# Optimization experiments

Measured on AMD Instinct MI355X. Metric: run time of the kernel, lower is better.

## Reference

```python
import jax, jax.numpy as jnp
import numpy as np

HEAD_SIZE = 64
TOKEN_EMB = 768
BLOCK_SIZE = 4096


def setup_inputs() -> dict:
    key = jax.random.key(0)
    ks = jax.random.split(key, 7)
    s = 1.0 / np.sqrt(TOKEN_EMB)  # torch Linear default init scale
    x = jax.random.normal(ks[0], (4, BLOCK_SIZE, TOKEN_EMB), dtype=jnp.float32)
    Wk = jax.random.uniform(ks[1], (TOKEN_EMB, HEAD_SIZE), minval=-s, maxval=s, dtype=jnp.float32)
    bk = jax.random.uniform(ks[2], (HEAD_SIZE,), minval=-s, maxval=s, dtype=jnp.float32)
    Wq = jax.random.uniform(ks[3], (TOKEN_EMB, HEAD_SIZE), minval=-s, maxval=s, dtype=jnp.float32)
    bq = jax.random.uniform(ks[4], (HEAD_SIZE,), minval=-s, maxval=s, dtype=jnp.float32)
    Wv = jax.random.uniform(ks[5], (TOKEN_EMB, HEAD_SIZE), minval=-s, maxval=s, dtype=jnp.float32)
    bv = jax.random.uniform(ks[6], (HEAD_SIZE,), minval=-s, maxval=s, dtype=jnp.float32)
    return {"x": x, "Wk": Wk, "bk": bk, "Wq": Wq, "bq": bq, "Wv": Wv, "bv": bv}


def reference(x, Wk, bk, Wq, bq, Wv, bv):
    B, T, C = x.shape
    k = x @ Wk + bk  # [B, T, H]
    q = x @ Wq + bq  # [B, T, H]
    v = x @ Wv + bv  # [B, T, H]
    # NOTE: original computes k @ q^T (not q @ k^T) and scales by C**-0.5 with
    # C = token embedding size (not head size). Reproduce faithfully.
    scale = jnp.asarray(C, x.dtype) ** -0.5
    wei = jnp.einsum('bth,bsh->bts', k, q) * scale  # [B, T, T]
    causal = jnp.tril(jnp.ones((T, T), dtype=bool))
    wei = jnp.where(causal, wei, -jnp.inf)
    wei = jax.nn.softmax(wei, axis=-1)
    return jnp.einsum('bts,bsh->bth', wei, v)  # [B, T, H]
```

## Files before the change

kernel.cpp:

```cpp
#include <hip/hip_runtime.h>
#include <hip/hip_bf16.h>

#define T_SEQ 4096
#define C_EMB 768
#define HEAD  64

typedef short  short4v __attribute__((ext_vector_type(4)));
typedef short  short8  __attribute__((ext_vector_type(8)));
typedef float  floatx4 __attribute__((ext_vector_type(4)));
typedef unsigned int uint2v __attribute__((ext_vector_type(2)));

static __device__ __forceinline__ short f2bf(float v) {
    __hip_bfloat16 h = __float2bfloat16(v);
    return *reinterpret_cast<short*>(&h);
}


__global__ void wt_transpose_kernel(const float* __restrict__ Wk,
                                    const float* __restrict__ Wq,
                                    const float* __restrict__ Wv,
                                    short* __restrict__ Wf) {
    const int total = 12 * 24 * 64 * 8;
    for (int idx = blockIdx.x * blockDim.x + threadIdx.x; idx < total;
         idx += gridDim.x * blockDim.x) {
        int e    = idx & 7;
        int lane = (idx >> 3) & 63;
        int t    = idx >> 9;
        int kc   = t % 24;
        int j    = t / 24;
        int g    = j >> 2;
        int n    = (j & 3) * 16 + (lane & 15);
        int k    = kc * 32 + ((lane >> 4) & 3) * 8 + e;
        const float* W = (g == 0) ? Wk : (g == 1) ? Wq : Wv;
        Wf[idx] = f2bf(W[k * HEAD + n]);
    }
}

__global__ __launch_bounds__(256) void qkv_mfma(
    const float* __restrict__ x, const short* __restrict__ Wf,
    const float* __restrict__ bkp, const float* __restrict__ bqp,
    const float* __restrict__ bvp,
    short* __restrict__ Kf, short* __restrict__ Qf, short* __restrict__ Vf) {
    const float scale2 = 0.052058773f;
    __shared__ __align__(16) short xs[32][200];

    const int tid  = threadIdx.x;
    const int w    = tid >> 6;
    const int lane = tid & 63;
    const int ln15 = lane & 15, quad = lane >> 4;
    const int rows0 = blockIdx.x * 32;
    const int rw = (w & 1) * 16;
    const int jb = (w >> 1) * 6;

    floatx4 acc[6];
#pragma unroll
    for (int jj = 0; jj < 6; ++jj) acc[jj] = (floatx4){0.f, 0.f, 0.f, 0.f};

    for (int ch = 0; ch < 4; ++ch) {
        floatx4 stg[6];
#pragma unroll
        for (int i = 0; i < 6; ++i) {
            int o   = i * 1024 + tid * 4;
            int r   = o / 192;
            int col = o - r * 192;
            stg[i] = *(const floatx4*)(x + (size_t)(rows0 + r) * C_EMB +
                                       ch * 192 + col);
        }
#pragma unroll
        for (int i = 0; i < 6; ++i) {
            int o   = i * 1024 + tid * 4;
            int r   = o / 192;
            int col = o - r * 192;
            unsigned p01, p23;
            asm("v_cvt_pk_bf16_f32 %0, %1, %2" : "=v"(p01) : "v"(stg[i][0]), "v"(stg[i][1]));
            asm("v_cvt_pk_bf16_f32 %0, %1, %2" : "=v"(p23) : "v"(stg[i][2]), "v"(stg[i][3]));
            *(uint2v*)&xs[r][col] = (uint2v){p01, p23};
        }
        __syncthreads();

#pragma unroll
        for (int kc2 = 0; kc2 < 6; ++kc2) {
            int kcg = ch * 6 + kc2;
            short8 a = *(const short8*)&xs[rw + ln15][kc2 * 32 + quad * 8];
            short8 wf[6];
#pragma unroll
            for (int jj = 0; jj < 6; ++jj)
                wf[jj] = *(const short8*)(Wf +
                    ((size_t)((jb + jj) * 24 + kcg) * 64 + lane) * 8);
#pragma unroll
            for (int jj = 0; jj < 6; ++jj)
                acc[jj] = __builtin_amdgcn_mfma_f32_16x16x32_bf16(a, wf[jj], acc[jj], 0, 0, 0);
        }
        __syncthreads();
    }

    short* lds = &xs[0][0];
#pragma unroll
    for (int jj = 0; jj < 6; ++jj) {
        int j  = jb + jj;
        int g  = j >> 2;
        int nl = (j & 3) * 16 + ln15;
        float bias = (g == 0 ? bkp : g == 1 ? bqp : bvp)[nl];
#pragma unroll
        for (int r = 0; r < 4; ++r) {
            int rloc = rw + quad * 4 + r;
            float v = acc[jj][r] + bias;
            int off;
            short val;
            if (g == 2) {
                val = f2bf(v);
                off = 4096 + ((nl >> 4) << 9) +
                      ((((rloc >> 3) & 3) << 4) | (nl & 15)) * 8 + (rloc & 7);
            } else {
                val = (g == 0) ? f2bf(v * scale2) : f2bf(v);
                int tr = rloc & 15, kh = nl >> 5;
                int hq = (nl >> 3) & 3, he = nl & 7;
                off = (g << 11) + (((rloc >> 4) * 2 + kh) << 9) +
                      (tr | (hq << 4)) * 8 + he;
            }
            lds[off] = val;
        }
    }
    __syncthreads();

    {
        int bb = rows0 >> 12, s = rows0 & 4095;
        size_t vbase = ((size_t)bb << 18) +
                       ((size_t)((s >> 6) * 8 + ((s >> 5) & 1)) << 9);
#pragma unroll
        for (int cc = 0; cc < 3; ++cc) {
            int i = (cc * 256 + tid) * 8;
            short8 d = *(const short8*)&lds[i];
            if (i < 2048)
                *(short8*)(Kf + (size_t)rows0 * 64 + i) = d;
            else if (i < 4096)
                *(short8*)(Qf + (size_t)rows0 * 64 + (i - 2048)) = d;
            else {
                int iv = i - 4096;
                *(short8*)(Vf + vbase + (size_t)(iv >> 9) * 1024 + (iv & 511)) = d;
            }
        }
    }
}

__global__ __launch_bounds__(64) void attn_part(
    const short* __restrict__ Kf, const short* __restrict__ Qf,
    const short* __restrict__ Vf, float* __restrict__ Opart,
    float* __restrict__ lpart) {
    __shared__ __align__(16) short Ps[32][72];

    int lane = threadIdx.x & 63;
    int ln15 = lane & 15, quad = lane >> 4;
    int g32 = blockIdx.x, c = blockIdx.y, b = blockIdx.z;
    int dtile = g32 >> 1;
    int lo = c * 8;
    if (lo > dtile) return;
    int hi = min(dtile, lo + 7);
    int base = g32 * 32;

    short8 bk[2][2];
    {
        const short* kfp = Kf + ((size_t)(b * 256 + g32 * 2) * 2) * 512 + lane * 8;
#pragma unroll
        for (int tg = 0; tg < 2; ++tg)
#pragma unroll
            for (int kh = 0; kh < 2; ++kh)
                bk[tg][kh] = *(const short8*)(kfp + (tg * 2 + kh) * 512);
    }

    floatx4 o[2][4];
#pragma unroll
    for (int tg = 0; tg < 2; ++tg)
#pragma unroll
        for (int hb = 0; hb < 4; ++hb) o[tg][hb] = (floatx4){0.f, 0.f, 0.f, 0.f};
    float ls[2] = {0.f, 0.f};

    const short* qfp = Qf + ((size_t)(b * 256 + lo * 4) * 2) * 512 + lane * 8;
    const short* vfp = Vf + ((size_t)b << 18) + (size_t)lo * 8 * 512 + lane * 8;

    short8 aqA[4][2], bvA[4][2], aqB[4][2], bvB[4][2];
#pragma unroll
    for (int sb = 0; sb < 4; ++sb)
#pragma unroll
        for (int kh = 0; kh < 2; ++kh)
            aqA[sb][kh] = *(const short8*)(qfp + (sb * 2 + kh) * 512);
#pragma unroll
    for (int hb = 0; hb < 4; ++hb)
#pragma unroll
        for (int kh = 0; kh < 2; ++kh)
            bvA[hb][kh] = *(const short8*)(vfp + (hb * 2 + kh) * 512);

    auto tile_step = [&](short8 (&aq)[4][2], short8 (&bv)[4][2],
                         short8 (&aqn)[4][2], short8 (&bvn)[4][2], int st) {
        if (st < hi) {
            int ti = st + 1 - lo;
#pragma unroll
            for (int sb = 0; sb < 4; ++sb)
#pragma unroll
                for (int kh = 0; kh < 2; ++kh)
                    aqn[sb][kh] = *(const short8*)(qfp + (size_t)ti * 4096 +
                                                   (sb * 2 + kh) * 512);
#pragma unroll
            for (int hb = 0; hb < 4; ++hb)
#pragma unroll
                for (int kh = 0; kh < 2; ++kh)
                    bvn[hb][kh] = *(const short8*)(vfp + (size_t)ti * 4096 +
                                                   (hb * 2 + kh) * 512);
        }

        floatx4 sacc[4][2];
#pragma unroll
        for (int sb = 0; sb < 4; ++sb)
#pragma unroll
            for (int tg = 0; tg < 2; ++tg) {
                floatx4 z = (floatx4){0.f, 0.f, 0.f, 0.f};
                z = __builtin_amdgcn_mfma_f32_16x16x32_bf16(aq[sb][0], bk[tg][0], z, 0, 0, 0);
                z = __builtin_amdgcn_mfma_f32_16x16x32_bf16(aq[sb][1], bk[tg][1], z, 0, 0, 0);
                sacc[sb][tg] = z;
            }

        bool diag = (st == dtile);
        int s0 = st * 64;
#pragma unroll
        for (int tg = 0; tg < 2; ++tg) {
            int tgl = base + tg * 16 + ln15;
#pragma unroll
            for (int sb = 0; sb < 4; ++sb) {
                float pv[4];
#pragma unroll
                for (int r = 0; r < 4; ++r) {
                    float p = __builtin_amdgcn_exp2f(sacc[sb][tg][r]);
                    if (diag) {
                        int sg = s0 + sb * 16 + quad * 4 + r;
                        p = (sg > tgl) ? 0.f : p;
                    }
                    pv[r] = p;
                }
                ls[tg] += (pv[0] + pv[1]) + (pv[2] + pv[3]);
                unsigned a01, a23;
                asm("v_cvt_pk_bf16_f32 %0, %1, %2" : "=v"(a01) : "v"(pv[0]), "v"(pv[1]));
                asm("v_cvt_pk_bf16_f32 %0, %1, %2" : "=v"(a23) : "v"(pv[2]), "v"(pv[3]));
                *(uint2v*)&Ps[tg * 16 + ln15][sb * 16 + quad * 4] = (uint2v){a01, a23};
            }
        }
        __asm__ volatile("s_waitcnt lgkmcnt(0)" ::: "memory");
        short8 ap[2][2];
#pragma unroll
        for (int tg = 0; tg < 2; ++tg) {
            ap[tg][0] = *(const short8*)&Ps[tg * 16 + ln15][quad * 8];
            ap[tg][1] = *(const short8*)&Ps[tg * 16 + ln15][32 + quad * 8];
        }

#pragma unroll
        for (int tg = 0; tg < 2; ++tg)
#pragma unroll
            for (int hb = 0; hb < 4; ++hb) {
                o[tg][hb] = __builtin_amdgcn_mfma_f32_16x16x32_bf16(ap[tg][0], bv[hb][0], o[tg][hb], 0, 0, 0);
                o[tg][hb] = __builtin_amdgcn_mfma_f32_16x16x32_bf16(ap[tg][1], bv[hb][1], o[tg][hb], 0, 0, 0);
            }
    };

#pragma unroll
    for (int it = 0; it < 8; it += 2) {
        if (lo + it > hi) break;
        tile_step(aqA, bvA, aqB, bvB, lo + it);
        if (lo + it + 1 > hi) break;
        tile_step(aqB, bvB, aqA, bvA, lo + it + 1);
    }

    float* op = Opart + ((size_t)(b * 8 + c) << 12) * HEAD;
    float* lp = lpart + ((size_t)(b * 8 + c) << 12);

#pragma unroll
    for (int tg = 0; tg < 2; ++tg) {
        float v = ls[tg];
        v += __shfl_xor(v, 16, 64);
        v += __shfl_xor(v, 32, 64);
        if (quad == 0)
            lp[base + tg * 16 + ln15] = v;
    }
#pragma unroll
    for (int tg = 0; tg < 2; ++tg)
#pragma unroll
        for (int r = 0; r < 4; ++r) {
            int t = base + tg * 16 + quad * 4 + r;
#pragma unroll
            for (int hb = 0; hb < 4; ++hb)
                op[(size_t)t * HEAD + hb * 16 + ln15] = o[tg][hb][r];
        }
}

__global__ __launch_bounds__(256) void attn_div(
    const float* __restrict__ Opart, const float* __restrict__ lpart,
    float* __restrict__ out) {
    int idx = blockIdx.x * 256 + threadIdx.x;
    int h = idx & 63;
    int t = (idx >> 6) & 4095;
    int b = idx >> 18;
    int nch = (t >> 9) + 1;
    float os = 0.f, l = 0.f;
    for (int c = 0; c < nch; ++c) {
        size_t s = (size_t)(b * 8 + c) << 12;
        os += Opart[(s + t) * HEAD + h];
        l  += lpart[s + t];
    }
    out[idx] = os / l;
}

extern "C" void kernel_launch(void* const* d_in, const int* in_sizes, int n_in,
                              void* d_out, int out_size, void* d_ws, size_t ws_size,
                              hipStream_t stream) {
    const int XSZ = 4 * T_SEQ * C_EMB;
    const int WSZ = C_EMB * HEAD;
    const int BSZ = HEAD;
    const float* x = nullptr;
    const float* W[3] = {nullptr, nullptr, nullptr};
    const float* B[3] = {nullptr, nullptr, nullptr};
    int iw = 0, ib = 0;
    for (int i = 0; i < n_in; ++i) {
        if (in_sizes[i] == XSZ) x = (const float*)d_in[i];
        else if (in_sizes[i] == WSZ && iw < 3) W[iw++] = (const float*)d_in[i];
        else if (in_sizes[i] == BSZ && ib < 3) B[ib++] = (const float*)d_in[i];
    }

    short* ws = (short*)d_ws;
    short* Kf = ws;
    short* Qf = Kf + (size_t)4 * T_SEQ * HEAD;
    short* Vf = Qf + (size_t)4 * T_SEQ * HEAD;
    short* Wf = Vf + (size_t)4 * HEAD * T_SEQ;
    float* Opart = (float*)(Wf + (size_t)3 * HEAD * C_EMB);
    float* lpart = Opart + (size_t)32 * T_SEQ * HEAD;

    wt_transpose_kernel<<<96, 256, 0, stream>>>(W[0], W[1], W[2], Wf);
    qkv_mfma<<<512, 256, 0, stream>>>(x, Wf, B[0], B[1], B[2], Kf, Qf, Vf);
    attn_part<<<dim3(128, 8, 4), 64, 0, stream>>>(Kf, Qf, Vf, Opart, lpart);
    attn_div<<<4096, 256, 0, stream>>>(Opart, lpart, (float*)d_out);
}
```

Before: 150.1 us.

## Widen QKV projection block to 512 threads and stage full x rows in LDS

The QKV projection kernel now runs 8 waves per block instead of 4, each computing 3 output column tiles rather than 6. It loads the whole 32x768 x tile into LDS in one pass instead of four 192-column chunks, which removes the per-chunk barriers, and then runs a single 24-step MFMA loop. The goal is more memory-level parallelism and latency hiding in the projection stage. In exchange, each block uses roughly 50KB of LDS, which can reduce the number of blocks resident per CU. A variable in the attention kernel is renamed with no effect on behaviour.

```diff
diff --git a/kernel.cpp b/kernel.cpp
--- a/kernel.cpp
+++ b/kernel.cpp
@@ -36,13 +36,13 @@
     }
 }
 
-__global__ __launch_bounds__(256) void qkv_mfma(
+__global__ __launch_bounds__(512) void qkv_mfma(
     const float* __restrict__ x, const short* __restrict__ Wf,
     const float* __restrict__ bkp, const float* __restrict__ bqp,
     const float* __restrict__ bvp,
     short* __restrict__ Kf, short* __restrict__ Qf, short* __restrict__ Vf) {
     const float scale2 = 0.052058773f;
-    __shared__ __align__(16) short xs[32][200];
+    __shared__ __align__(16) short xs[32][776];
 
     const int tid  = threadIdx.x;
     const int w    = tid >> 6;
@@ -50,53 +50,54 @@
     const int ln15 = lane & 15, quad = lane >> 4;
     const int rows0 = blockIdx.x * 32;
     const int rw = (w & 1) * 16;
-    const int jb = (w >> 1) * 6;
-
-    floatx4 acc[6];
-#pragma unroll
-    for (int jj = 0; jj < 6; ++jj) acc[jj] = (floatx4){0.f, 0.f, 0.f, 0.f};
-
-    for (int ch = 0; ch < 4; ++ch) {
+    const int jb = (w >> 1) * 3;
+
+#pragma unroll
+    for (int grp = 0; grp < 2; ++grp) {
         floatx4 stg[6];
 #pragma unroll
         for (int i = 0; i < 6; ++i) {
-            int o   = i * 1024 + tid * 4;
-            int r   = o / 192;
-            int col = o - r * 192;
-            stg[i] = *(const floatx4*)(x + (size_t)(rows0 + r) * C_EMB +
-                                       ch * 192 + col);
+            int o = (grp * 6 + i) * 2048 + tid * 4;
+            int r = o / 768, col = o - r * 768;
+            stg[i] = *(const floatx4*)(x + (size_t)(rows0 + r) * C_EMB + col);
         }
 #pragma unroll
         for (int i = 0; i < 6; ++i) {
-            int o   = i * 1024 + tid * 4;
-            int r   = o / 192;
-            int col = o - r * 192;
+            int o = (grp * 6 + i) * 2048 + tid * 4;
+            int r = o / 768, col = o - r * 768;
             unsigned p01, p23;
             asm("v_cvt_pk_bf16_f32 %0, %1, %2" : "=v"(p01) : "v"(stg[i][0]), "v"(stg[i][1]));
             asm("v_cvt_pk_bf16_f32 %0, %1, %2" : "=v"(p23) : "v"(stg[i][2]), "v"(stg[i][3]));
             *(uint2v*)&xs[r][col] = (uint2v){p01, p23};
         }
-        __syncthreads();
-
-#pragma unroll
-        for (int kc2 = 0; kc2 < 6; ++kc2) {
-            int kcg = ch * 6 + kc2;
-            short8 a = *(const short8*)&xs[rw + ln15][kc2 * 32 + quad * 8];
-            short8 wf[6];
-#pragma unroll
-            for (int jj = 0; jj < 6; ++jj)
-                wf[jj] = *(const short8*)(Wf +
-                    ((size_t)((jb + jj) * 24 + kcg) * 64 + lane) * 8);
-#pragma unroll
-            for (int jj = 0; jj < 6; ++jj)
-                acc[jj] = __builtin_amdgcn_mfma_f32_16x16x32_bf16(a, wf[jj], acc[jj], 0, 0, 0);
-        }
-        __syncthreads();
-    }
+    }
+    __syncthreads();
+
+    const short* wp[3];
+#pragma unroll
+    for (int j0 = 0; j0 < 3; ++j0)
+        wp[j0] = Wf + ((size_t)((jb + j0) * 24) * 64 + lane) * 8;
+
+    floatx4 acc[3];
+#pragma unroll
+    for (int jj = 0; jj < 3; ++jj) acc[jj] = (floatx4){0.f, 0.f, 0.f, 0.f};
+
+#pragma unroll
+    for (int kc = 0; kc < 24; ++kc) {
+        short8 a = *(const short8*)&xs[rw + ln15][kc * 32 + quad * 8];
+        short8 wf[3];
+#pragma unroll
+        for (int jj = 0; jj < 3; ++jj)
+            wf[jj] = *(const short8*)(wp[jj] + kc * 512);
+#pragma unroll
+        for (int jj = 0; jj < 3; ++jj)
+            acc[jj] = __builtin_amdgcn_mfma_f32_16x16x32_bf16(a, wf[jj], acc[jj], 0, 0, 0);
+    }
+    __syncthreads();
 
     short* lds = &xs[0][0];
 #pragma unroll
-    for (int jj = 0; jj < 6; ++jj) {
+    for (int jj = 0; jj < 3; ++jj) {
         int j  = jb + jj;
         int g  = j >> 2;
         int nl = (j & 3) * 16 + ln15;
@@ -128,16 +129,18 @@
         size_t vbase = ((size_t)bb << 18) +
                        ((size_t)((s >> 6) * 8 + ((s >> 5) & 1)) << 9);
 #pragma unroll
-        for (int cc = 0; cc < 3; ++cc) {
-            int i = (cc * 256 + tid) * 8;
-            short8 d = *(const short8*)&lds[i];
-            if (i < 2048)
-                *(short8*)(Kf + (size_t)rows0 * 64 + i) = d;
-            else if (i < 4096)
-                *(short8*)(Qf + (size_t)rows0 * 64 + (i - 2048)) = d;
-            else {
-                int iv = i - 4096;
-                *(short8*)(Vf + vbase + (size_t)(iv >> 9) * 1024 + (iv & 511)) = d;
+        for (int cc = 0; cc < 2; ++cc) {
+            int i = (cc * 512 + tid) * 8;
+            if (i < 6144) {
+                short8 d = *(const short8*)&lds[i];
+                if (i < 2048)
+                    *(short8*)(Kf + (size_t)rows0 * 64 + i) = d;
+                else if (i < 4096)
+                    *(short8*)(Qf + (size_t)rows0 * 64 + (i - 2048)) = d;
+                else {
+                    int iv = i - 4096;
+                    *(short8*)(Vf + vbase + (size_t)(iv >> 9) * 1024 + (iv & 511)) = d;
+                }
             }
         }
     }
@@ -226,7 +229,7 @@
             int tgl = base + tg * 16 + ln15;
 #pragma unroll
             for (int sb = 0; sb < 4; ++sb) {
-                float pv[4];
+                float pv4[4];
 #pragma unroll
                 for (int r = 0; r < 4; ++r) {
                     float p = __builtin_amdgcn_exp2f(sacc[sb][tg][r]);
@@ -234,12 +237,12 @@
                         int sg = s0 + sb * 16 + quad * 4 + r;
                         p = (sg > tgl) ? 0.f : p;
                     }
-                    pv[r] = p;
+                    pv4[r] = p;
                 }
-                ls[tg] += (pv[0] + pv[1]) + (pv[2] + pv[3]);
+                ls[tg] += (pv4[0] + pv4[1]) + (pv4[2] + pv4[3]);
                 unsigned a01, a23;
-                asm("v_cvt_pk_bf16_f32 %0, %1, %2" : "=v"(a01) : "v"(pv[0]), "v"(pv[1]));
-                asm("v_cvt_pk_bf16_f32 %0, %1, %2" : "=v"(a23) : "v"(pv[2]), "v"(pv[3]));
+                asm("v_cvt_pk_bf16_f32 %0, %1, %2" : "=v"(a01) : "v"(pv4[0]), "v"(pv4[1]));
+                asm("v_cvt_pk_bf16_f32 %0, %1, %2" : "=v"(a23) : "v"(pv4[2]), "v"(pv4[3]));
                 *(uint2v*)&Ps[tg * 16 + ln15][sb * 16 + quad * 4] = (uint2v){a01, a23};
             }
         }
@@ -332,7 +335,7 @@
     float* lpart = Opart + (size_t)32 * T_SEQ * HEAD;
 
     wt_transpose_kernel<<<96, 256, 0, stream>>>(W[0], W[1], W[2], Wf);
-    qkv_mfma<<<512, 256, 0, stream>>>(x, Wf, B[0], B[1], B[2], Kf, Qf, Vf);
+    qkv_mfma<<<512, 512, 0, stream>>>(x, Wf, B[0], B[1], B[2], Kf, Qf, Vf);
     attn_part<<<dim3(128, 8, 4), 64, 0, stream>>>(Kf, Qf, Vf, Opart, lpart);
     attn_div<<<4096, 256, 0, stream>>>(Opart, lpart, (float*)d_out);
 }
```

Result: faster. 142.2 us (-5.2%).
